# Optimization experiments

Hardware: AMD Instinct MI355X
Metric: run time of the kernel (lower is better)

## Reference

```python
import jax, jax.numpy as jnp
import numpy as np

B, S, D, H = 2, 2048, 768, 12
DK = D // H


def setup_inputs() -> dict:
    key = jax.random.key(0)
    ks = jax.random.split(key, 12)
    inp = {
        "q": jax.random.normal(ks[0], (B, S, D), jnp.float32),
        "k": jax.random.normal(ks[1], (B, S, D), jnp.float32),
        "v": jax.random.normal(ks[2], (B, S, D), jnp.float32),
        # float mask: 1.0 where attention is disallowed (causal upper triangle)
        "mask": (1.0 - jnp.tril(jnp.ones((S, S), jnp.float32)))[None, None],
        "Wq": jax.random.normal(ks[3], (D, D), jnp.float32) / np.sqrt(D),
        "bq": jnp.zeros((D,), jnp.float32),
        "Wk": jax.random.normal(ks[4], (D, D), jnp.float32) / np.sqrt(D),
        "bk": jnp.zeros((D,), jnp.float32),
        "Wv": jax.random.normal(ks[5], (D, D), jnp.float32) / np.sqrt(D),
        "bv": jnp.zeros((D,), jnp.float32),
        "Wo": jax.random.normal(ks[6], (D, D), jnp.float32) / np.sqrt(D),
        "bo": jnp.zeros((D,), jnp.float32),
    }
    return inp


def _split_heads(x):
    # [B,S,D] -> [B,H,S,DK]
    b, s, _ = x.shape
    return x.reshape(b, s, H, DK).transpose(0, 2, 1, 3)


def reference(q, k, v, mask, Wq, bq, Wk, bk, Wv, bv, Wo, bo):
    Q = _split_heads(q @ Wq + bq)
    K = _split_heads(k @ Wk + bk)
    V = _split_heads(v @ Wv + bv)
    scale = jax.lax.rsqrt(jnp.float32(D))  # note: d_model, not d_k (faithful)
    logits = jnp.einsum("bhqd,bhkd->bhqk", Q, K) * scale
    logits = logits + (-1e9) * mask
    weights = jax.nn.softmax(logits, axis=-1)
    attn = jnp.einsum("bhqk,bhkd->bhqd", weights, V)
    attn = attn.transpose(0, 2, 1, 3).reshape(q.shape)  # [B,S,D]
    return jax.nn.relu(attn @ Wo + bo)
```

## Files before the change

kernel.cpp:

```cpp
#include <hip/hip_runtime.h>
#include <math.h>

#define BB 2
#define SS 2048
#define DD 768
#define HH 12
#define DKK 64
#define MM (BB*SS)

typedef _Float16 half_t;
using half8 = __attribute__((ext_vector_type(8))) _Float16;
using half4 = __attribute__((ext_vector_type(4))) _Float16;
using floatx4 = __attribute__((ext_vector_type(4))) float;

__global__ __launch_bounds__(256)
void prep(const float* __restrict__ q, const float* __restrict__ k,
          const float* __restrict__ v,
          const float* __restrict__ Wq, const float* __restrict__ Wk,
          const float* __restrict__ Wv, const float* __restrict__ Wo,
          half_t* __restrict__ qh, half_t* __restrict__ kh,
          half_t* __restrict__ vh,
          half_t* __restrict__ Wqt, half_t* __restrict__ Wkt,
          half_t* __restrict__ Wvt, half_t* __restrict__ Wot)
{
    __shared__ float tile[64][68];
    const int y = blockIdx.y;
    const int t = threadIdx.x;
    if (y < 3) {
        const float* src = y == 0 ? q : (y == 1 ? k : v);
        half_t* dst      = y == 0 ? qh : (y == 1 ? kh : vh);
        int i = blockIdx.x * 256 + t;
        float4 f = ((const float4*)src)[i];
        half4 hv;
        hv[0] = (half_t)f.x; hv[1] = (half_t)f.y;
        hv[2] = (half_t)f.z; hv[3] = (half_t)f.w;
        ((half4*)dst)[i] = hv;
    } else {
        int x = blockIdx.x;
        if (x >= 576) return;
        int w = x / 144, rem = x % 144;
        const float* W = w == 0 ? Wq : w == 1 ? Wk : w == 2 ? Wv : Wo;
        half_t* T      = w == 0 ? Wqt : w == 1 ? Wkt : w == 2 ? Wvt : Wot;
        int k0 = (rem % 12) * 64, n0 = (rem / 12) * 64;
        #pragma unroll
        for (int i = 0; i < 4; ++i) {
            int c = t + i * 256;
            int kr = c >> 4, nc = (c & 15) * 4;
            *(float4*)&tile[kr][nc] = *(const float4*)&W[(size_t)(k0 + kr) * DD + n0 + nc];
        }
        __syncthreads();
        #pragma unroll
        for (int i = 0; i < 4; ++i) {
            int c = t + i * 256;
            int nr = c >> 4, kc = (c & 15) * 4;
            half4 hv;
            #pragma unroll
            for (int jj = 0; jj < 4; ++jj) hv[jj] = (half_t)tile[kc + jj][nr];
            *(half4*)&T[(size_t)(n0 + nr) * DD + k0 + kc] = hv;
        }
    }
}

template<bool SWAP>
__device__ __forceinline__
void gemm_body(const half_t* __restrict__ A, const half_t* __restrict__ Bt,
               floatx4 (&acc)[4][2], half_t (*As)[72], half_t (*Bs)[72],
               int m0, int n0)
{
    const int t = threadIdx.x;
    const int lane = t & 63, wave = t >> 6;
    const int lr = lane & 15, lq = lane >> 4;
    const int wm = (wave >> 1) * 64, wn = (wave & 1) * 32;
    const int a_r = t >> 1,  a_c = (t & 1) * 32;
    const int b_r = t >> 2,  b_c = (t & 3) * 16;

    #pragma unroll
    for (int mi = 0; mi < 4; ++mi)
        #pragma unroll
        for (int ni = 0; ni < 2; ++ni)
            #pragma unroll
            for (int r = 0; r < 4; ++r) acc[mi][ni][r] = 0.f;

    for (int k0 = 0; k0 < DD; k0 += 64) {
        __syncthreads();
        #pragma unroll
        for (int jj = 0; jj < 4; ++jj)
            *(half8*)&As[a_r][a_c + jj * 8] =
                *(const half8*)&A[(size_t)(m0 + a_r) * DD + k0 + a_c + jj * 8];
        #pragma unroll
        for (int jj = 0; jj < 2; ++jj)
            *(half8*)&Bs[b_r][b_c + jj * 8] =
                *(const half8*)&Bt[(size_t)(n0 + b_r) * DD + k0 + b_c + jj * 8];
        __syncthreads();

        half8 af[4][2], bf[2][2];
        #pragma unroll
        for (int mi = 0; mi < 4; ++mi)
            #pragma unroll
            for (int kp = 0; kp < 2; ++kp)
                af[mi][kp] = *(const half8*)&As[wm + mi * 16 + lr][kp * 32 + lq * 8];
        #pragma unroll
        for (int ni = 0; ni < 2; ++ni)
            #pragma unroll
            for (int kp = 0; kp < 2; ++kp)
                bf[ni][kp] = *(const half8*)&Bs[wn + ni * 16 + lr][kp * 32 + lq * 8];

        #pragma unroll
        for (int mi = 0; mi < 4; ++mi)
            #pragma unroll
            for (int ni = 0; ni < 2; ++ni)
                #pragma unroll
                for (int kp = 0; kp < 2; ++kp) {
                    if (SWAP)
                        acc[mi][ni] = __builtin_amdgcn_mfma_f32_16x16x32_f16(
                            bf[ni][kp], af[mi][kp], acc[mi][ni], 0, 0, 0);
                    else
                        acc[mi][ni] = __builtin_amdgcn_mfma_f32_16x16x32_f16(
                            af[mi][kp], bf[ni][kp], acc[mi][ni], 0, 0, 0);
                }
    }
}

__device__ __forceinline__ void xcd_decode(int bx, int& m0, int& n0)
{
    int xcd = bx & 7, g = bx >> 3;
    m0 = (xcd * 4 + g / 12) * 128;
    n0 = (g % 12) * 64;
}

__global__ __launch_bounds__(256)
void proj_gemm(const half_t* __restrict__ qh, const half_t* __restrict__ kh,
               const half_t* __restrict__ vh,
               const half_t* __restrict__ Wqt, const half_t* __restrict__ Wkt,
               const half_t* __restrict__ Wvt,
               const float* __restrict__ bq, const float* __restrict__ bk,
               const float* __restrict__ bv,
               half_t* __restrict__ Qo, half_t* __restrict__ Ko,
               half_t* __restrict__ Vto)
{
    const int z = blockIdx.z;
    const half_t* A  = z == 0 ? qh  : z == 1 ? kh  : vh;
    const half_t* Bt = z == 0 ? Wqt : z == 1 ? Wkt : Wvt;
    const float* bias = z == 0 ? bq : z == 1 ? bk : bv;

    __shared__ half_t As[128][72];
    __shared__ half_t Bs[64][72];
    floatx4 acc[4][2];
    int m0, n0;
    xcd_decode(blockIdx.x, m0, n0);

    if (z == 2) gemm_body<true >(A, Bt, acc, As, Bs, m0, n0);
    else        gemm_body<false>(A, Bt, acc, As, Bs, m0, n0);

    const int lane = threadIdx.x & 63, wave = threadIdx.x >> 6;
    const int lr = lane & 15, lq = lane >> 4;
    const int wm = (wave >> 1) * 64, wn = (wave & 1) * 32;

    if (z == 2) {
        #pragma unroll
        for (int mi = 0; mi < 4; ++mi)
            #pragma unroll
            for (int ni = 0; ni < 2; ++ni)
                #pragma unroll
                for (int r = 0; r < 4; ++r) {
                    int dcol = n0 + wn + ni * 16 + lq * 4 + r;
                    int srow = m0 + wm + mi * 16 + lr;
                    int hh = dcol >> 6, d = dcol & 63;
                    int b2 = srow >> 11, sdx = srow & 2047;
                    Vto[((size_t)((b2 * HH + hh) * DKK + d)) * SS + sdx] =
                        (half_t)(acc[mi][ni][r] + bias[dcol]);
                }
    } else {
        const float sc = (z == 0) ? 0.03608439182435161f : 1.0f;
        half_t* O = z == 0 ? Qo : Ko;
        #pragma unroll
        for (int mi = 0; mi < 4; ++mi)
            #pragma unroll
            for (int ni = 0; ni < 2; ++ni)
                #pragma unroll
                for (int r = 0; r < 4; ++r) {
                    int row = m0 + wm + mi * 16 + lq * 4 + r;
                    int col = n0 + wn + ni * 16 + lr;
                    O[(size_t)row * DD + col] = (half_t)((acc[mi][ni][r] + bias[col]) * sc);
                }
    }
}

__global__ __launch_bounds__(256)
void out_gemm(const half_t* __restrict__ A, const half_t* __restrict__ Bt,
              const float* __restrict__ bias, float* __restrict__ C)
{
    __shared__ half_t As[128][72];
    __shared__ half_t Bs[64][72];
    floatx4 acc[4][2];
    int m0, n0;
    xcd_decode(blockIdx.x, m0, n0);
    gemm_body<false>(A, Bt, acc, As, Bs, m0, n0);

    const int lane = threadIdx.x & 63, wave = threadIdx.x >> 6;
    const int lr = lane & 15, lq = lane >> 4;
    const int wm = (wave >> 1) * 64, wn = (wave & 1) * 32;

    #pragma unroll
    for (int mi = 0; mi < 4; ++mi)
        #pragma unroll
        for (int ni = 0; ni < 2; ++ni)
            #pragma unroll
            for (int r = 0; r < 4; ++r) {
                int row = m0 + wm + mi * 16 + lq * 4 + r;
                int col = n0 + wn + ni * 16 + lr;
                C[(size_t)row * DD + col] = fmaxf(acc[mi][ni][r] + bias[col], 0.f);
            }
}

__device__ const int QT_TAB[40] = {3,4,5,6,7,7,8,8,9,9,10,10,11,11,11,12,12,12,
                                   13,13,13,14,14,14,15,15,15,15,
                                   2,6,10,14, 1,5,9,13, 0,4,8,12};
__device__ const int C_TAB[40]  = {0,0,0,0,0,1,0,1,0,1,0,1,0,1,2,0,1,2,
                                   0,1,2,0,1,2,0,1,2,3,
                                   0,1,2,3, 0,1,2,3, 0,1,2,3};

__global__ __launch_bounds__(256)
void attn_split(const half_t* __restrict__ Qf, const half_t* __restrict__ Kf,
                const half_t* __restrict__ Vt, half_t* __restrict__ Of,
                half_t* __restrict__ Opart, float* __restrict__ Lpart)
{
    __shared__ half_t Ks[64][72];
    __shared__ half_t Vs[64][72];
    __shared__ half_t Ps[4][32][72];

    const int i = blockIdx.x;
    const int bh = i % 24;
    const int j = i / 24;
    const int qt = QT_TAB[j];
    const int c  = C_TAB[j];
    const bool single = (qt <= 3);
    const int kt0 = c * 8;
    const int iters = 2 * qt + 2;
    const int kt1 = (kt0 + 8 < iters) ? (kt0 + 8) : iters;

    const int b = bh / HH, h = bh % HH;
    const int t = threadIdx.x;
    const int lane = t & 63, wave = t >> 6;
    const int lr = lane & 15, lq = lane >> 4;
    const int q0 = qt * 128;

    const int srow = t >> 3;
    const int scol = (t & 7) * 8;

    const half_t* Kbase = Kf + (size_t)(b * SS) * DD + h * DKK;
    const half_t* Vbase = Vt + (size_t)((b * HH + h) * DKK) * SS;

    half8 kpre[2], vpre[2];
    #pragma unroll
    for (int ii = 0; ii < 2; ++ii) {
        int row = srow + ii * 32;
        kpre[ii] = *(const half8*)&Kbase[(size_t)(kt0 * 64 + row) * DD + scol];
        vpre[ii] = *(const half8*)&Vbase[(size_t)row * SS + kt0 * 64 + scol];
    }

    half8 qa[2][2];
    #pragma unroll
    for (int qg = 0; qg < 2; ++qg) {
        const half_t* qptr =
            Qf + (size_t)(b * SS + q0 + wave * 32 + qg * 16 + lr) * DD + h * DKK;
        qa[qg][0] = *(const half8*)(qptr + lq * 8);
        qa[qg][1] = *(const half8*)(qptr + 32 + lq * 8);
    }

    floatx4 o[2][4];
    #pragma unroll
    for (int qg = 0; qg < 2; ++qg)
        #pragma unroll
        for (int nt = 0; nt < 4; ++nt)
            #pragma unroll
            for (int r = 0; r < 4; ++r) o[qg][nt][r] = 0.f;
    float l_run[2] = {0.f, 0.f};

    for (int kt = kt0; kt < kt1; ++kt) {
        __syncthreads();
        #pragma unroll
        for (int ii = 0; ii < 2; ++ii) {
            int row = srow + ii * 32;
            *(half8*)&Ks[row][scol] = kpre[ii];
            *(half8*)&Vs[row][scol] = vpre[ii];
        }
        __syncthreads();

        if (kt + 1 < kt1) {
            #pragma unroll
            for (int ii = 0; ii < 2; ++ii) {
                int row = srow + ii * 32;
                kpre[ii] = *(const half8*)&Kbase[(size_t)((kt + 1) * 64 + row) * DD + scol];
                vpre[ii] = *(const half8*)&Vbase[(size_t)row * SS + (kt + 1) * 64 + scol];
            }
        }

        floatx4 s[2][4];
        #pragma unroll
        for (int nt = 0; nt < 4; ++nt) {
            half8 kf0 = *(const half8*)&Ks[nt * 16 + lr][lq * 8];
            half8 kf1 = *(const half8*)&Ks[nt * 16 + lr][32 + lq * 8];
            #pragma unroll
            for (int qg = 0; qg < 2; ++qg) {
                floatx4 a = {0.f, 0.f, 0.f, 0.f};
                a = __builtin_amdgcn_mfma_f32_16x16x32_f16(kf0, qa[qg][0], a, 0, 0, 0);
                a = __builtin_amdgcn_mfma_f32_16x16x32_f16(kf1, qa[qg][1], a, 0, 0, 0);
                s[qg][nt] = a;
            }
        }

        if (kt >= 2 * qt) {
            #pragma unroll
            for (int qg = 0; qg < 2; ++qg) {
                int qrow = q0 + wave * 32 + qg * 16 + lr;
                #pragma unroll
                for (int nt = 0; nt < 4; ++nt)
                    #pragma unroll
                    for (int r = 0; r < 4; ++r) {
                        int key = kt * 64 + nt * 16 + lq * 4 + r;
                        if (key > qrow) s[qg][nt][r] = -1e30f;
                    }
            }
        }

        #pragma unroll
        for (int qg = 0; qg < 2; ++qg)
            #pragma unroll
            for (int nt = 0; nt < 4; ++nt) {
                half4 hp;
                #pragma unroll
                for (int r = 0; r < 4; ++r) {
                    float p = __expf(s[qg][nt][r]);
                    l_run[qg] += p;
                    hp[r] = (half_t)p;
                }
                *(half4*)&Ps[wave][qg * 16 + lr][nt * 16 + lq * 4] = hp;
            }

        __builtin_amdgcn_s_waitcnt(0xc07f);

        half8 pa[2][2];
        #pragma unroll
        for (int qg = 0; qg < 2; ++qg) {
            pa[qg][0] = *(const half8*)&Ps[wave][qg * 16 + lr][lq * 8];
            pa[qg][1] = *(const half8*)&Ps[wave][qg * 16 + lr][32 + lq * 8];
        }

        #pragma unroll
        for (int nt = 0; nt < 4; ++nt) {
            half8 vf0 = *(const half8*)&Vs[nt * 16 + lr][lq * 8];
            half8 vf1 = *(const half8*)&Vs[nt * 16 + lr][32 + lq * 8];
            #pragma unroll
            for (int qg = 0; qg < 2; ++qg) {
                o[qg][nt] = __builtin_amdgcn_mfma_f32_16x16x32_f16(vf0, pa[qg][0], o[qg][nt], 0, 0, 0);
                o[qg][nt] = __builtin_amdgcn_mfma_f32_16x16x32_f16(vf1, pa[qg][1], o[qg][nt], 0, 0, 0);
            }
        }
    }

    #pragma unroll
    for (int qg = 0; qg < 2; ++qg) {
        l_run[qg] += __shfl_xor(l_run[qg], 16);
        l_run[qg] += __shfl_xor(l_run[qg], 32);
    }

    if (single) {
        #pragma unroll
        for (int qg = 0; qg < 2; ++qg) {
            float inv = 1.f / l_run[qg];
            int qrow = q0 + wave * 32 + qg * 16 + lr;
            #pragma unroll
            for (int nt = 0; nt < 4; ++nt) {
                half4 hv;
                #pragma unroll
                for (int r = 0; r < 4; ++r) hv[r] = (half_t)(o[qg][nt][r] * inv);
                *(half4*)&Of[(size_t)(b * SS + qrow) * DD + h * DKK + nt * 16 + lq * 4] = hv;
            }
        }
    } else {
        const int p = (bh * 12 + (qt - 4)) * 4 + c;
        half_t* Ob = Opart + (size_t)p * 8192;
        #pragma unroll
        for (int qg = 0; qg < 2; ++qg) {
            int qq = wave * 32 + qg * 16 + lr;
            #pragma unroll
            for (int nt = 0; nt < 4; ++nt) {
                half4 hv;
                #pragma unroll
                for (int r = 0; r < 4; ++r) hv[r] = (half_t)o[qg][nt][r];
                *(half4*)&Ob[qq * 64 + nt * 16 + lq * 4] = hv;
            }
            if (lq == 0) Lpart[p * 128 + qq] = l_run[qg];
        }
    }
}

__global__ __launch_bounds__(256)
void attn_combine(const half_t* __restrict__ Opart, const float* __restrict__ Lpart,
                  half_t* __restrict__ Of)
{
    const int ib = blockIdx.x;
    const int bh = ib / 12, qtm = ib % 12;
    const int qt = qtm + 4;
    const int nc = (2 * qt + 9) / 8;
    const int b = bh / HH, h = bh % HH;
    const int pbase = (bh * 12 + qtm) * 4;
    const int t = threadIdx.x;
    const int qq = t >> 1, ds0 = (t & 1) * 32;

    float l = 0.f;
    for (int cc = 0; cc < nc; ++cc) l += Lpart[(pbase + cc) * 128 + qq];
    const float inv = 1.f / l;

    float accv[32];
    #pragma unroll
    for (int e = 0; e < 32; ++e) accv[e] = 0.f;
    for (int cc = 0; cc < nc; ++cc) {
        const half_t* Os = Opart + (size_t)(pbase + cc) * 8192 + qq * 64 + ds0;
        #pragma unroll
        for (int kk = 0; kk < 4; ++kk) {
            half8 x = *(const half8*)&Os[kk * 8];
            #pragma unroll
            for (int e = 0; e < 8; ++e) accv[kk * 8 + e] += (float)x[e];
        }
    }

    int srow = qt * 128 + qq;
    half_t* dst = Of + (size_t)(b * SS + srow) * DD + h * DKK + ds0;
    #pragma unroll
    for (int kk = 0; kk < 8; ++kk) {
        half4 hv;
        hv[0] = (half_t)(accv[kk * 4 + 0] * inv);
        hv[1] = (half_t)(accv[kk * 4 + 1] * inv);
        hv[2] = (half_t)(accv[kk * 4 + 2] * inv);
        hv[3] = (half_t)(accv[kk * 4 + 3] * inv);
        *(half4*)&dst[kk * 4] = hv;
    }
}

extern "C" void kernel_launch(void* const* d_in, const int* in_sizes, int n_in,
                              void* d_out, int out_size, void* d_ws, size_t ws_size,
                              hipStream_t stream)
{
    (void)in_sizes; (void)n_in; (void)out_size; (void)ws_size;
    const float* q  = (const float*)d_in[0];
    const float* k  = (const float*)d_in[1];
    const float* v  = (const float*)d_in[2];
    const float* Wq = (const float*)d_in[4];
    const float* bq = (const float*)d_in[5];
    const float* Wk = (const float*)d_in[6];
    const float* bk = (const float*)d_in[7];
    const float* Wv = (const float*)d_in[8];
    const float* bv = (const float*)d_in[9];
    const float* Wo = (const float*)d_in[10];
    const float* bo = (const float*)d_in[11];
    float* out = (float*)d_out;

    half_t* qh  = (half_t*)d_ws;
    half_t* kh  = qh  + (size_t)MM * DD;
    half_t* vh  = kh  + (size_t)MM * DD;
    half_t* Wqt = vh  + (size_t)MM * DD;
    half_t* Wkt = Wqt + (size_t)DD * DD;
    half_t* Wvt = Wkt + (size_t)DD * DD;
    half_t* Wot = Wvt + (size_t)DD * DD;
    half_t* Qo  = Wot + (size_t)DD * DD;
    half_t* Ko  = Qo  + (size_t)MM * DD;
    half_t* Vto = Ko  + (size_t)MM * DD;
    half_t* Ao  = Vto + (size_t)MM * DD;
    half_t* Opart = Ao + (size_t)MM * DD;
    float*  Lpart = (float*)(Opart + (size_t)1152 * 8192);

    prep<<<dim3(3072, 4), 256, 0, stream>>>(q, k, v, Wq, Wk, Wv, Wo,
                                            qh, kh, vh, Wqt, Wkt, Wvt, Wot);
    proj_gemm<<<dim3(384, 1, 3), 256, 0, stream>>>(
        qh, kh, vh, Wqt, Wkt, Wvt, bq, bk, bv, Qo, Ko, Vto);
    attn_split<<<dim3(24 * 40), 256, 0, stream>>>(Qo, Ko, Vto, Ao, Opart, Lpart);
    attn_combine<<<dim3(288), 256, 0, stream>>>(Opart, Lpart, Ao);
    out_gemm<<<dim3(384), 256, 0, stream>>>(Ao, Wot, bo, out);
}
```

Baseline: 194.5 us.

## Fuse split-KV attention combine into output projection GEMM A-tile load

New measurement: 224.1 us. 15.2% more time.

```diff
diff --git a/kernel.cpp b/kernel.cpp
--- a/kernel.cpp
+++ b/kernel.cpp
@@ -187,19 +187,108 @@
 }
 
 __global__ __launch_bounds__(256)
-void out_gemm(const half_t* __restrict__ A, const half_t* __restrict__ Bt,
+void out_gemm(const half_t* __restrict__ Ao, const half_t* __restrict__ Opart,
+              const float* __restrict__ Lpart, const half_t* __restrict__ Bt,
               const float* __restrict__ bias, float* __restrict__ C)
 {
     __shared__ half_t As[128][72];
     __shared__ half_t Bs[64][72];
-    floatx4 acc[4][2];
+    __shared__ float invl[HH][128];
+
+    const int t = threadIdx.x;
     int m0, n0;
     xcd_decode(blockIdx.x, m0, n0);
-    gemm_body<false>(A, Bt, acc, As, Bs, m0, n0);
-
-    const int lane = threadIdx.x & 63, wave = threadIdx.x >> 6;
+    const int mtile = m0 >> 7;
+    const int bb = mtile >> 4;
+    const int qt = mtile & 15;
+    const bool split = (qt >= 4);
+    const int nc = (2 * qt + 9) >> 3;
+
+    if (split) {
+        for (int idx = t; idx < HH * 128; idx += 256) {
+            int h = idx >> 7, qq = idx & 127;
+            int pb = ((bb * HH + h) * 12 + (qt - 4)) * 4;
+            float l = 0.f;
+            for (int cc = 0; cc < nc; ++cc) l += Lpart[(pb + cc) * 128 + qq];
+            invl[h][qq] = 1.f / l;
+        }
+    }
+
+    const int lane = t & 63, wave = t >> 6;
     const int lr = lane & 15, lq = lane >> 4;
     const int wm = (wave >> 1) * 64, wn = (wave & 1) * 32;
+    const int a_r = t >> 1,  a_c = (t & 1) * 32;
+    const int b_r = t >> 2,  b_c = (t & 3) * 16;
+
+    floatx4 acc[4][2];
+    #pragma unroll
+    for (int mi = 0; mi < 4; ++mi)
+        #pragma unroll
+        for (int ni = 0; ni < 2; ++ni)
+            #pragma unroll
+            for (int r = 0; r < 4; ++r) acc[mi][ni][r] = 0.f;
+
+    for (int k0 = 0; k0 < DD; k0 += 64) {
+        __syncthreads();
+        if (!split) {
+            #pragma unroll
+            for (int jj = 0; jj < 4; ++jj)
+                *(half8*)&As[a_r][a_c + jj * 8] =
+                    *(const half8*)&Ao[(size_t)(m0 + a_r) * DD + k0 + a_c + jj * 8];
+        } else {
+            const int h = k0 >> 6;
+            const int pb = ((bb * HH + h) * 12 + (qt - 4)) * 4;
+            const float il = invl[h][a_r];
+            #pragma unroll
+            for (int jj = 0; jj < 2; ++jj) {
+                int d = a_c + jj * 16;
+                float accv[16];
+                #pragma unroll
+                for (int e = 0; e < 16; ++e) accv[e] = 0.f;
+                for (int cc = 0; cc < nc; ++cc) {
+                    const half_t* Os = Opart + (size_t)(pb + cc) * 8192 + a_r * 64 + d;
+                    half8 x0 = *(const half8*)Os;
+                    half8 x1 = *(const half8*)(Os + 8);
+                    #pragma unroll
+                    for (int e = 0; e < 8; ++e) { accv[e] += (float)x0[e]; accv[8 + e] += (float)x1[e]; }
+                }
+                half8 h0, h1;
+                #pragma unroll
+                for (int e = 0; e < 8; ++e) {
+                    h0[e] = (half_t)(accv[e] * il);
+                    h1[e] = (half_t)(accv[8 + e] * il);
+                }
+                *(half8*)&As[a_r][d] = h0;
+                *(half8*)&As[a_r][d + 8] = h1;
+            }
+        }
+        #pragma unroll
+        for (int jj = 0; jj < 2; ++jj)
+            *(half8*)&Bs[b_r][b_c + jj * 8] =
+                *(const half8*)&Bt[(size_t)(n0 + b_r) * DD + k0 + b_c + jj * 8];
+        __syncthreads();
+
+        half8 af[4][2], bf[2][2];
+        #pragma unroll
+        for (int mi = 0; mi < 4; ++mi)
+            #pragma unroll
+            for (int kp = 0; kp < 2; ++kp)
+                af[mi][kp] = *(const half8*)&As[wm + mi * 16 + lr][kp * 32 + lq * 8];
+        #pragma unroll
+        for (int ni = 0; ni < 2; ++ni)
+            #pragma unroll
+            for (int kp = 0; kp < 2; ++kp)
+                bf[ni][kp] = *(const half8*)&Bs[wn + ni * 16 + lr][kp * 32 + lq * 8];
+
+        #pragma unroll
+        for (int mi = 0; mi < 4; ++mi)
+            #pragma unroll
+            for (int ni = 0; ni < 2; ++ni)
+                #pragma unroll
+                for (int kp = 0; kp < 2; ++kp)
+                    acc[mi][ni] = __builtin_amdgcn_mfma_f32_16x16x32_f16(
+                        af[mi][kp], bf[ni][kp], acc[mi][ni], 0, 0, 0);
+    }
 
     #pragma unroll
     for (int mi = 0; mi < 4; ++mi)
@@ -393,49 +482,6 @@
             }
             if (lq == 0) Lpart[p * 128 + qq] = l_run[qg];
         }
-    }
-}
-
-__global__ __launch_bounds__(256)
-void attn_combine(const half_t* __restrict__ Opart, const float* __restrict__ Lpart,
-                  half_t* __restrict__ Of)
-{
-    const int ib = blockIdx.x;
-    const int bh = ib / 12, qtm = ib % 12;
-    const int qt = qtm + 4;
-    const int nc = (2 * qt + 9) / 8;
-    const int b = bh / HH, h = bh % HH;
-    const int pbase = (bh * 12 + qtm) * 4;
-    const int t = threadIdx.x;
-    const int qq = t >> 1, ds0 = (t & 1) * 32;
-
-    float l = 0.f;
-    for (int cc = 0; cc < nc; ++cc) l += Lpart[(pbase + cc) * 128 + qq];
-    const float inv = 1.f / l;
-
-    float accv[32];
-    #pragma unroll
-    for (int e = 0; e < 32; ++e) accv[e] = 0.f;
-    for (int cc = 0; cc < nc; ++cc) {
-        const half_t* Os = Opart + (size_t)(pbase + cc) * 8192 + qq * 64 + ds0;
-        #pragma unroll
-        for (int kk = 0; kk < 4; ++kk) {
-            half8 x = *(const half8*)&Os[kk * 8];
-            #pragma unroll
-            for (int e = 0; e < 8; ++e) accv[kk * 8 + e] += (float)x[e];
-        }
-    }
-
-    int srow = qt * 128 + qq;
-    half_t* dst = Of + (size_t)(b * SS + srow) * DD + h * DKK + ds0;
-    #pragma unroll
-    for (int kk = 0; kk < 8; ++kk) {
-        half4 hv;
-        hv[0] = (half_t)(accv[kk * 4 + 0] * inv);
-        hv[1] = (half_t)(accv[kk * 4 + 1] * inv);
-        hv[2] = (half_t)(accv[kk * 4 + 2] * inv);
-        hv[3] = (half_t)(accv[kk * 4 + 3] * inv);
-        *(half4*)&dst[kk * 4] = hv;
     }
 }
 
@@ -476,6 +522,5 @@
     proj_gemm<<<dim3(384, 1, 3), 256, 0, stream>>>(
         qh, kh, vh, Wqt, Wkt, Wvt, bq, bk, bv, Qo, Ko, Vto);
     attn_split<<<dim3(24 * 40), 256, 0, stream>>>(Qo, Ko, Vto, Ao, Opart, Lpart);
-    attn_combine<<<dim3(288), 256, 0, stream>>>(Opart, Lpart, Ao);
-    out_gemm<<<dim3(384), 256, 0, stream>>>(Ao, Wot, bo, out);
-}
+    out_gemm<<<dim3(384), 256, 0, stream>>>(Ao, Opart, Lpart, Wot, bo, out);
+}
```
